# Kernel optimization log

Hardware: AMD Instinct MI355X
Metric: run time of the kernel (lower is better)

Reference implementation:

```python
import jax, jax.numpy as jnp
import numpy as np

B, S, T = 256, 1024, 64

def setup_inputs() -> dict:
    key = jax.random.key(0)
    k1, k2, k3, k4, k5 = jax.random.split(key, 5)
    emissions = jax.random.normal(k1, (B, S, T), dtype=jnp.float32)
    tags = jax.random.randint(k2, (B, S), 0, T, dtype=jnp.int64)
    mask = jnp.ones((B, S), dtype=jnp.int32)
    transitions = jax.random.normal(k3, (T, T), dtype=jnp.float32) * 0.1
    start_transitions = jax.random.normal(k4, (T,), dtype=jnp.float32) * 0.1
    end_transitions = jax.random.normal(k5, (T,), dtype=jnp.float32) * 0.1
    return {"emissions": emissions, "tags": tags, "mask": mask,
            "transitions": transitions, "start_transitions": start_transitions,
            "end_transitions": end_transitions}


def _gold_score(emissions, tags, maskf, transitions, start_transitions, end_transitions):
    # emission score at each gold tag: [B, S]
    emit = jnp.take_along_axis(emissions, tags[:, :, None], axis=2)[:, :, 0]
    # transition score between consecutive gold tags: [B, S-1]
    trans = transitions[tags[:, :-1], tags[:, 1:]]
    score = start_transitions[tags[:, 0]] + emit[:, 0]
    score = score + jnp.sum((trans + emit[:, 1:]) * maskf[:, 1:], axis=1)
    last_pos = maskf.astype(jnp.int32).sum(axis=1) - 1           # [B]
    last_tags = jnp.take_along_axis(tags, last_pos[:, None], axis=1)[:, 0]
    return score + end_transitions[last_tags]


def _log_partition(emissions, maskf, transitions, start_transitions, end_transitions):
    alpha0 = start_transitions[None, :] + emissions[:, 0]        # [B, T]

    def step(alpha, xs):
        emit_t, m_t = xs                                         # [B, T], [B]
        # scores[b, i, j] = alpha[b, i] + transitions[i, j] + emit_t[b, j]
        scores = alpha[:, :, None] + transitions[None, :, :] + emit_t[:, None, :]
        new_alpha = jax.nn.logsumexp(scores, axis=1)             # [B, T]
        alpha = jnp.where(m_t[:, None] > 0, new_alpha, alpha)
        return alpha, None

    xs = (jnp.swapaxes(emissions[:, 1:], 0, 1), jnp.swapaxes(maskf[:, 1:], 0, 1))
    alpha, _ = jax.lax.scan(step, alpha0, xs)
    return jax.nn.logsumexp(alpha + end_transitions[None, :], axis=1)  # [B]


def reference(emissions, tags, mask, transitions, start_transitions, end_transitions):
    maskf = mask.astype(emissions.dtype)
    log_Z = _log_partition(emissions, maskf, transitions, start_transitions, end_transitions)
    score = _gold_score(emissions, tags, maskf, transitions, start_transitions, end_transitions)
    return jnp.mean(log_Z - score)
```

## Files before the change

### kernel.cpp

```cpp
#include <hip/hip_runtime.h>

#define Bn 256
#define Sn 1024
#define Tn 64
#define NCH 16
#define BURN 64
#define SLAB 4
#define RAWSTR 260
#define CROW 72
#define MROW 129
#define LN2 0.69314718055994531f
#define L7LN2 4.8520302639196169f

typedef __attribute__((ext_vector_type(8))) short short8;
typedef __attribute__((ext_vector_type(4))) float f32x4;

__device__ __forceinline__ unsigned short f2bf_rne(float f) {
  unsigned u = __float_as_uint(f);
  u = (u + 0x7fffu + ((u >> 16) & 1u)) >> 16;
  return (unsigned short)u;
}
__device__ __forceinline__ unsigned pk2(float hi, float lo) {
  return __builtin_amdgcn_perm(__float_as_uint(hi), __float_as_uint(lo), 0x07060302);
}
__device__ __forceinline__ unsigned pke(float a, float b) {
  return (unsigned)f2bf_rne(__expf(a - L7LN2)) |
         ((unsigned)f2bf_rne(__expf(b - L7LN2)) << 16);
}
__device__ __forceinline__ short8 cat4(uint2 a, uint2 b) {
  union { unsigned u[4]; short8 s; } x;
  x.u[0] = a.x; x.u[1] = a.y; x.u[2] = b.x; x.u[3] = b.y;
  return x.s;
}
__device__ __forceinline__ void gl_lds16(const void* src, void* dst) {
  __builtin_amdgcn_global_load_lds(
      (const __attribute__((address_space(1))) void*)src,
      (__attribute__((address_space(3))) void*)dst, 16, 0, 0);
}
__device__ __forceinline__ void gl_lds4(const void* src, void* dst) {
  __builtin_amdgcn_global_load_lds(
      (const __attribute__((address_space(1))) void*)src,
      (__attribute__((address_space(3))) void*)dst, 4, 0, 0);
}

__global__ __launch_bounds__(256, 1) void crf_scan(
    const float* __restrict__ em, const int* __restrict__ tags,
    const int* __restrict__ mask, const float* __restrict__ trans,
    const float* __restrict__ startt, const float* __restrict__ endt,
    float* __restrict__ wsL, float* __restrict__ wsGold,
    int* __restrict__ wsM, float* __restrict__ wsSE, float* __restrict__ wsA,
    int* __restrict__ cnt, float* __restrict__ out) {
  const int g = blockIdx.x & 15;
  const int c = blockIdx.x >> 4;
  const int Wc = (c == 0) ? 0 : BURN;
  const int Lc = (c == NCH - 1) ? 63 : 64;
  const int TOT = Wc + Lc;
  const int NSLAB = (TOT + SLAB - 1) / SLAB;
  const int t0 = 64 * c + 1;
  const int tstart = t0 - Wc;
  const int tid = threadIdx.x;
  const int wid = tid >> 6;
  const int lane = tid & 63;
  const int m = lane & 15;
  const int q = lane >> 4;
  const int mrow = 8 * (m >> 2) + (m & 3);

  __shared__ __align__(16) float rawS[2][16 * RAWSTR];
  __shared__ __align__(16) short convS[2][SLAB * 16 * CROW];
  __shared__ int maskL[16 * MROW];
  __shared__ int lastF;
  __shared__ float eend[64];
  __shared__ float rsum[4];

  short8 a00, a01, a10, a11, a20, a21, a30, a31;
  uint2 st0, st1, st2, st3;
  float Slog = 0.f;
  int K = 0, NL = 0;
  const f32x4 zero4 = {0.f, 0.f, 0.f, 0.f};

  auto issue_slab = [&](int s) {
    if (s >= NSLAB) return;
    float* dstb = rawS[s & 1];
    const int rem = TOT - 4 * s;
    if (rem >= SLAB) {
      for (int mm = 0; mm < 16; ++mm)
        gl_lds16(em + ((size_t)(16 * g + mm) * Sn + tstart + 4 * s) * 64 + lane * 4,
                 dstb + mm * RAWSTR);
    } else {
      for (int mm = 0; mm < 16; ++mm)
        for (int u = 0; u < rem; ++u)
          gl_lds4(em + ((size_t)(16 * g + mm) * Sn + tstart + 4 * s + u) * 64 + lane,
                  dstb + mm * RAWSTR + u * 64);
    }
  };
  auto conv_u = [&](const float* rp, short* cb, int mm, int base, int u) {
    float4 v0 = *(const float4*)(rp + u * 64 + 0);
    float4 v1 = *(const float4*)(rp + u * 64 + 4);
    float4 v2 = *(const float4*)(rp + u * 64 + 8);
    float4 v3 = *(const float4*)(rp + u * 64 + 12);
    uint4 o0, o1;
    o0.x = pke(v0.x, v0.y); o0.y = pke(v0.z, v0.w);
    o1.x = pke(v1.x, v1.y); o1.y = pke(v1.z, v1.w);
    o0.z = pke(v2.x, v2.y); o0.w = pke(v2.z, v2.w);
    o1.z = pke(v3.x, v3.y); o1.w = pke(v3.z, v3.w);
    short* cw = cb + (u * 16 + mm) * CROW + base;
    *(uint4*)(cw) = o0;
    *(uint4*)(cw + 16) = o1;
  };
  auto convert2 = [&](int s, int ua) {
    const int mm = lane & 15, seg = lane >> 4;
    const float* rp = rawS[s & 1] + mm * RAWSTR + seg * 16;
    short* cb = convS[s & 1];
    const int base = (seg >> 1) * 32 + (seg & 1) * 8;
    conv_u(rp, cb, mm, base, ua);
    conv_u(rp, cb, mm, base, ua + 1);
  };
  auto convert_tail2 = [&](int s, int ua) {
    if (s >= NSLAB) return;
    const int mm = lane & 15, seg = lane >> 4;
    const float* rp = rawS[s & 1] + mm * RAWSTR + seg * 16;
    short* cb = convS[s & 1];
    const int base = (seg >> 1) * 32 + (seg & 1) * 8;
    const int vu = min(SLAB, TOT - 4 * s);
    const int ub = min(vu, ua + 2);
    for (int u = ua; u < ub; ++u) conv_u(rp, cb, mm, base, u);
  };

  if (wid == 0) {
#define LOADA(tm, kc, dst) { \
    _Pragma("unroll") for (int jj = 0; jj < 8; ++jj) { \
      int kk = kc * 32 + q * 8 + jj; \
      dst[jj] = (short)f2bf_rne(__expf(trans[kk * Tn + (32 * ((tm) >> 1) + 4 * ((tm) & 1) + mrow)])); \
    } }
    LOADA(0, 0, a00) LOADA(0, 1, a01) LOADA(1, 0, a10) LOADA(1, 1, a11)
    LOADA(2, 0, a20) LOADA(2, 1, a21) LOADA(3, 0, a30) LOADA(3, 1, a31)
#undef LOADA
    if (c == 0) {
#define INIT0(off, ss) { \
      float4 sv = *(const float4*)(startt + (off)); \
      float4 ev = *(const float4*)(em + (size_t)(16 * g + m) * Sn * Tn + (off)); \
      ss.x = (unsigned)f2bf_rne(__expf(sv.x + ev.x)) | \
             ((unsigned)f2bf_rne(__expf(sv.y + ev.y)) << 16); \
      ss.y = (unsigned)f2bf_rne(__expf(sv.z + ev.z)) | \
             ((unsigned)f2bf_rne(__expf(sv.w + ev.w)) << 16); }
      INIT0(8 * q, st0) INIT0(8 * q + 4, st1)
      INIT0(32 + 8 * q, st2) INIT0(36 + 8 * q, st3)
#undef INIT0
    } else {
      st0.x = 0x3F803F80u; st0.y = 0x3F803F80u; st1 = st0; st2 = st0; st3 = st0;
    }
  } else if (wid == 1) {
    for (int mm = 0; mm < 16; ++mm) {
      gl_lds4(mask + (size_t)(16 * g + mm) * Sn + tstart + lane,
              (void*)(maskL + mm * MROW));
      bool special = (c == NCH - 1) && (g == 15) && (mm == 15);
      if (!special)
        gl_lds4(mask + (size_t)(16 * g + mm) * Sn + tstart + 64 + lane,
                (void*)(maskL + mm * MROW + 64));
    }
    if (c == NCH - 1 && g == 15) {
      int t = tstart + 64 + lane;
      if (t < Sn) maskL[15 * MROW + 64 + lane] = mask[(size_t)255 * Sn + t];
    }
    asm volatile("s_waitcnt vmcnt(0) lgkmcnt(0)" ::: "memory");
  } else if (wid == 2) {
    const int bm = 16 * g + m;
    const int qq = q;
    const int* tg = tags + (size_t)bm * Sn;
    const int* mkb = mask + (size_t)bm * Sn;
    const float* emb = em + (size_t)bm * Sn * Tn;
    float acc = 0.f;
    int cntg = 0;
    #pragma unroll 4
    for (int i = 0; i < 16; ++i) {
      int t = t0 + qq + 4 * i;
      bool ok = t < t0 + Lc;
      int ts = ok ? t : t0;
      int mv = mkb[ts];
      int tp = tg[ts - 1], tc = tg[ts];
      float w = trans[tp * Tn + tc] + emb[(size_t)ts * Tn + tc];
      acc += (ok && mv) ? w : 0.f;
      cntg += ok ? mv : 0;
    }
    acc += __shfl_xor(acc, 16); acc += __shfl_xor(acc, 32);
    cntg += __shfl_xor(cntg, 16); cntg += __shfl_xor(cntg, 32);
    if (qq == 0) { wsGold[c * 256 + bm] = acc; wsM[c * 256 + bm] = cntg; }
  } else {
    issue_slab(0);
    issue_slab(1);
    asm volatile("s_waitcnt vmcnt(0)" ::: "memory");
  }
  __syncthreads();

  if (wid == 1) convert2(0, 0);
  else if (wid == 2) convert2(0, 2);
  __syncthreads();

#define UNP(ss, x0, x1, x2, x3) \
  x0 = __uint_as_float(ss.x << 16); x1 = __uint_as_float(ss.x & 0xffff0000u); \
  x2 = __uint_as_float(ss.y << 16); x3 = __uint_as_float(ss.y & 0xffff0000u);

  auto renorm = [&](int ttz) {
    float x00, x01, x02, x03, x10, x11, x12, x13;
    float x20, x21, x22, x23, x30, x31, x32, x33;
    UNP(st0, x00, x01, x02, x03) UNP(st1, x10, x11, x12, x13)
    UNP(st2, x20, x21, x22, x23) UNP(st3, x30, x31, x32, x33)
    float sm = (((x00 + x01) + (x02 + x03)) + ((x10 + x11) + (x12 + x13)))
             + (((x20 + x21) + (x22 + x23)) + ((x30 + x31) + (x32 + x33)));
    sm += __shfl_xor(sm, 16); sm += __shfl_xor(sm, 32);
    if (c != 0 && ttz == BURN) { Slog = __logf(sm); K = 0; NL = 0; }
    int k = 127 - (int)((__float_as_uint(sm) >> 23) & 255u);
    float fk = __uint_as_float((unsigned)(127 + k) << 23);
    x00 *= fk; x01 *= fk; x02 *= fk; x03 *= fk;
    x10 *= fk; x11 *= fk; x12 *= fk; x13 *= fk;
    x20 *= fk; x21 *= fk; x22 *= fk; x23 *= fk;
    x30 *= fk; x31 *= fk; x32 *= fk; x33 *= fk;
    st0.x = pk2(x01, x00); st0.y = pk2(x03, x02);
    st1.x = pk2(x11, x10); st1.y = pk2(x13, x12);
    st2.x = pk2(x21, x20); st2.y = pk2(x23, x22);
    st3.x = pk2(x31, x30); st3.y = pk2(x33, x32);
    K += k;
  };

  auto scan_step = [&](const short* ep, int tt) {
    uint2 eu0 = *(const uint2*)(ep + 0 + 4 * q);
    uint2 eu1 = *(const uint2*)(ep + 16 + 4 * q);
    uint2 eu2 = *(const uint2*)(ep + 32 + 4 * q);
    uint2 eu3 = *(const uint2*)(ep + 48 + 4 * q);
    int mv = maskL[m * MROW + tt];
    short8 b0 = cat4(st0, st1);
    short8 b1 = cat4(st2, st3);
    f32x4 d0 = __builtin_amdgcn_mfma_f32_16x16x32_bf16(a00, b0, zero4, 0, 0, 0);
    f32x4 d1 = __builtin_amdgcn_mfma_f32_16x16x32_bf16(a10, b0, zero4, 0, 0, 0);
    f32x4 d2 = __builtin_amdgcn_mfma_f32_16x16x32_bf16(a20, b0, zero4, 0, 0, 0);
    f32x4 d3 = __builtin_amdgcn_mfma_f32_16x16x32_bf16(a30, b0, zero4, 0, 0, 0);
    d0 = __builtin_amdgcn_mfma_f32_16x16x32_bf16(a01, b1, d0, 0, 0, 0);
    d1 = __builtin_amdgcn_mfma_f32_16x16x32_bf16(a11, b1, d1, 0, 0, 0);
    d2 = __builtin_amdgcn_mfma_f32_16x16x32_bf16(a21, b1, d2, 0, 0, 0);
    d3 = __builtin_amdgcn_mfma_f32_16x16x32_bf16(a31, b1, d3, 0, 0, 0);
    const bool live = (mv != 0);
#define EPI(dd, eu, ss) { \
    float e0 = __uint_as_float(eu.x << 16); \
    float e1 = __uint_as_float(eu.x & 0xffff0000u); \
    float e2 = __uint_as_float(eu.y << 16); \
    float e3 = __uint_as_float(eu.y & 0xffff0000u); \
    unsigned nx = pk2(dd[1] * e1, dd[0] * e0); \
    unsigned ny = pk2(dd[3] * e3, dd[2] * e2); \
    ss.x = live ? nx : ss.x; \
    ss.y = live ? ny : ss.y; }
    EPI(d0, eu0, st0) EPI(d1, eu1, st1) EPI(d2, eu2, st2) EPI(d3, eu3, st3)
#undef EPI
    NL += (live && tt >= Wc) ? 1 : 0;
  };

  const int RT = (TOT - 4) >> 2;
  for (int r = 0; r < NSLAB; ++r) {
    if (wid == 0) {
      if ((r & 1) == 0) renorm(4 * r);
      const short* cbase = convS[r & 1];
      if (r < RT) {
        #pragma unroll
        for (int u = 0; u < SLAB; ++u)
          scan_step(cbase + (u * 16 + m) * CROW, 4 * r + u);
      } else {
        #pragma unroll
        for (int u = 0; u < SLAB; ++u)
          if (4 * r + u < TOT)
            scan_step(cbase + (u * 16 + m) * CROW, 4 * r + u);
      }
    } else if (wid == 3) {
      issue_slab(r + 2);
      asm volatile("s_waitcnt vmcnt(0)" ::: "memory");
    } else {
      const int ua = (wid == 1) ? 0 : 2;
      if (r < RT) convert2(r + 1, ua);
      else        convert_tail2(r + 1, ua);
    }
    __syncthreads();
  }

  if (wid == 0) {
    float x00, x01, x02, x03, x10, x11, x12, x13;
    float x20, x21, x22, x23, x30, x31, x32, x33;
    UNP(st0, x00, x01, x02, x03) UNP(st1, x10, x11, x12, x13)
    UNP(st2, x20, x21, x22, x23) UNP(st3, x30, x31, x32, x33)
    float sm = (((x00 + x01) + (x02 + x03)) + ((x10 + x11) + (x12 + x13)))
             + (((x20 + x21) + (x22 + x23)) + ((x30 + x31) + (x32 + x33)));
    sm += __shfl_xor(sm, 16); sm += __shfl_xor(sm, 32);
    const int bm = 16 * g + m;
    float L = __logf(sm) - Slog + LN2 * (float)(7 * NL - K);
    if (q == 0) wsL[c * 256 + bm] = L;
    if (c == NCH - 1) {
      if (q == 0) wsSE[bm] = __logf(sm);
      wsA[(8 * q + 0) * 256 + bm] = x00;  wsA[(8 * q + 1) * 256 + bm] = x01;
      wsA[(8 * q + 2) * 256 + bm] = x02;  wsA[(8 * q + 3) * 256 + bm] = x03;
      wsA[(8 * q + 4) * 256 + bm] = x10;  wsA[(8 * q + 5) * 256 + bm] = x11;
      wsA[(8 * q + 6) * 256 + bm] = x12;  wsA[(8 * q + 7) * 256 + bm] = x13;
      wsA[(32 + 8 * q + 0) * 256 + bm] = x20; wsA[(32 + 8 * q + 1) * 256 + bm] = x21;
      wsA[(32 + 8 * q + 2) * 256 + bm] = x22; wsA[(32 + 8 * q + 3) * 256 + bm] = x23;
      wsA[(36 + 8 * q + 0) * 256 + bm] = x30; wsA[(36 + 8 * q + 1) * 256 + bm] = x31;
      wsA[(36 + 8 * q + 2) * 256 + bm] = x32; wsA[(36 + 8 * q + 3) * 256 + bm] = x33;
    }
  }
#undef UNP

  __threadfence();
  __syncthreads();
  if (tid == 0) lastF = (atomicAdd(cnt, 1) == 255) ? 1 : 0;
  __syncthreads();
  if (lastF) {
    __threadfence();
    if (tid < 64) eend[tid] = __expf(endt[tid]);
    __syncthreads();
    float vsum = 0.f;
    for (int bb = tid; bb < Bn; bb += 256) {
      float sumL = 0.f, gold = 0.f;
      int msum = 0;
      #pragma unroll
      for (int cc = 0; cc < NCH; ++cc) {
        sumL += wsL[cc * 256 + bb];
        gold += wsGold[cc * 256 + bb];
        msum += wsM[cc * 256 + bb];
      }
      msum += mask[(size_t)bb * Sn];
      float se = 0.f;
      for (int jj = 0; jj < Tn; ++jj) se += wsA[jj * 256 + bb] * eend[jj];
      float logZ = sumL + __logf(se) - wsSE[bb];
      int tg0 = tags[(size_t)bb * Sn];
      int lastTag = tags[(size_t)bb * Sn + (msum - 1)];
      gold += startt[tg0] + em[(size_t)bb * Sn * Tn + tg0] + endt[lastTag];
      vsum += logZ - gold;
    }
    #pragma unroll
    for (int o = 32; o > 0; o >>= 1) vsum += __shfl_xor(vsum, o, 64);
    if (lane == 0) rsum[wid] = vsum;
    __syncthreads();
    if (tid == 0) out[0] = (rsum[0] + rsum[1] + rsum[2] + rsum[3]) * (1.0f / Bn);
  }
}

extern "C" void kernel_launch(void* const* d_in, const int* in_sizes, int n_in,
                              void* d_out, int out_size, void* d_ws, size_t ws_size,
                              hipStream_t stream) {
  const float* em     = (const float*)d_in[0];
  const int*   tags   = (const int*)d_in[1];
  const int*   mask   = (const int*)d_in[2];
  const float* trans  = (const float*)d_in[3];
  const float* startt = (const float*)d_in[4];
  const float* endt   = (const float*)d_in[5];
  float* out = (float*)d_out;

  float* wsL    = (float*)d_ws;
  float* wsGold = wsL + NCH * 256;
  int*   wsM    = (int*)(wsGold + NCH * 256);
  float* wsSE   = (float*)(wsM + NCH * 256);
  float* wsA    = wsSE + 256;
  int*   cnt    = (int*)(wsA + 64 * 256);

  hipMemsetAsync(cnt, 0, sizeof(int), stream);
  crf_scan<<<256, 256, 0, stream>>>(em, tags, mask, trans, startt, endt,
                                    wsL, wsGold, wsM, wsSE, wsA, cnt, out);
}
```

Before: 163.1 us.

## Deepen emission prefetch to four raw slabs split across three loader waves

Raw emission staging grows from two to four LDS buffers, and the global-to-LDS loads are now split by row across waves 1-3 instead of coming only from wave 3. Loads are issued three slabs ahead and throttled with partial vmcnt waits, so several slabs stay in flight instead of draining to zero each step. The per-step __syncthreads is replaced with a raw s_barrier to avoid its implicit full wait. This raises LDS usage and depends on hand-counted vmcnt values being correct. It also drops the separate tail convert, which may convert rows past the valid timesteps in the final slab.

Result: no change. 163.9 us (+0.5%).

```diff
diff --git a/kernel.cpp b/kernel.cpp
--- a/kernel.cpp
+++ b/kernel.cpp
@@ -65,7 +65,7 @@
   const int q = lane >> 4;
   const int mrow = 8 * (m >> 2) + (m & 3);
 
-  __shared__ __align__(16) float rawS[2][16 * RAWSTR];
+  __shared__ __align__(16) float rawS[4][16 * RAWSTR];
   __shared__ __align__(16) short convS[2][SLAB * 16 * CROW];
   __shared__ int maskL[16 * MROW];
   __shared__ int lastF;
@@ -78,16 +78,16 @@
   int K = 0, NL = 0;
   const f32x4 zero4 = {0.f, 0.f, 0.f, 0.f};
 
-  auto issue_slab = [&](int s) {
+  auto issue_rows = [&](int s, int mm0, int mm1) {
     if (s >= NSLAB) return;
-    float* dstb = rawS[s & 1];
+    float* dstb = rawS[s & 3];
     const int rem = TOT - 4 * s;
     if (rem >= SLAB) {
-      for (int mm = 0; mm < 16; ++mm)
+      for (int mm = mm0; mm < mm1; ++mm)
         gl_lds16(em + ((size_t)(16 * g + mm) * Sn + tstart + 4 * s) * 64 + lane * 4,
                  dstb + mm * RAWSTR);
     } else {
-      for (int mm = 0; mm < 16; ++mm)
+      for (int mm = mm0; mm < mm1; ++mm)
         for (int u = 0; u < rem; ++u)
           gl_lds4(em + ((size_t)(16 * g + mm) * Sn + tstart + 4 * s + u) * 64 + lane,
                   dstb + mm * RAWSTR + u * 64);
@@ -108,22 +108,13 @@
     *(uint4*)(cw + 16) = o1;
   };
   auto convert2 = [&](int s, int ua) {
+    if (s >= NSLAB) return;
     const int mm = lane & 15, seg = lane >> 4;
-    const float* rp = rawS[s & 1] + mm * RAWSTR + seg * 16;
+    const float* rp = rawS[s & 3] + mm * RAWSTR + seg * 16;
     short* cb = convS[s & 1];
     const int base = (seg >> 1) * 32 + (seg & 1) * 8;
     conv_u(rp, cb, mm, base, ua);
     conv_u(rp, cb, mm, base, ua + 1);
-  };
-  auto convert_tail2 = [&](int s, int ua) {
-    if (s >= NSLAB) return;
-    const int mm = lane & 15, seg = lane >> 4;
-    const float* rp = rawS[s & 1] + mm * RAWSTR + seg * 16;
-    short* cb = convS[s & 1];
-    const int base = (seg >> 1) * 32 + (seg & 1) * 8;
-    const int vu = min(SLAB, TOT - 4 * s);
-    const int ub = min(vu, ua + 2);
-    for (int u = ua; u < ub; ++u) conv_u(rp, cb, mm, base, u);
   };
 
   if (wid == 0) {
@@ -150,6 +141,33 @@
       st0.x = 0x3F803F80u; st0.y = 0x3F803F80u; st1 = st0; st2 = st0; st3 = st0;
     }
   } else if (wid == 1) {
+    issue_rows(0, 0, 6); issue_rows(1, 0, 6); issue_rows(2, 0, 6);
+    asm volatile("s_waitcnt vmcnt(0)" ::: "memory");
+  } else if (wid == 2) {
+    issue_rows(0, 6, 12); issue_rows(1, 6, 12); issue_rows(2, 6, 12);
+    const int bm = 16 * g + m;
+    const int* tg = tags + (size_t)bm * Sn;
+    const int* mkb = mask + (size_t)bm * Sn;
+    const float* emb = em + (size_t)bm * Sn * Tn;
+    float acc = 0.f;
+    int cntg = 0;
+    #pragma unroll 4
+    for (int i = 0; i < 16; ++i) {
+      int t = t0 + q + 4 * i;
+      bool ok = t < t0 + Lc;
+      int ts = ok ? t : t0;
+      int mv = mkb[ts];
+      int tp = tg[ts - 1], tc = tg[ts];
+      float w = trans[tp * Tn + tc] + emb[(size_t)ts * Tn + tc];
+      acc += (ok && mv) ? w : 0.f;
+      cntg += ok ? mv : 0;
+    }
+    acc += __shfl_xor(acc, 16); acc += __shfl_xor(acc, 32);
+    cntg += __shfl_xor(cntg, 16); cntg += __shfl_xor(cntg, 32);
+    if (q == 0) { wsGold[c * 256 + bm] = acc; wsM[c * 256 + bm] = cntg; }
+    asm volatile("s_waitcnt vmcnt(0)" ::: "memory");
+  } else {
+    issue_rows(0, 12, 16); issue_rows(1, 12, 16); issue_rows(2, 12, 16);
     for (int mm = 0; mm < 16; ++mm) {
       gl_lds4(mask + (size_t)(16 * g + mm) * Sn + tstart + lane,
               (void*)(maskL + mm * MROW));
@@ -163,32 +181,6 @@
       if (t < Sn) maskL[15 * MROW + 64 + lane] = mask[(size_t)255 * Sn + t];
     }
     asm volatile("s_waitcnt vmcnt(0) lgkmcnt(0)" ::: "memory");
-  } else if (wid == 2) {
-    const int bm = 16 * g + m;
-    const int qq = q;
-    const int* tg = tags + (size_t)bm * Sn;
-    const int* mkb = mask + (size_t)bm * Sn;
-    const float* emb = em + (size_t)bm * Sn * Tn;
-    float acc = 0.f;
-    int cntg = 0;
-    #pragma unroll 4
-    for (int i = 0; i < 16; ++i) {
-      int t = t0 + qq + 4 * i;
-      bool ok = t < t0 + Lc;
-      int ts = ok ? t : t0;
-      int mv = mkb[ts];
-      int tp = tg[ts - 1], tc = tg[ts];
-      float w = trans[tp * Tn + tc] + emb[(size_t)ts * Tn + tc];
-      acc += (ok && mv) ? w : 0.f;
-      cntg += ok ? mv : 0;
-    }
-    acc += __shfl_xor(acc, 16); acc += __shfl_xor(acc, 32);
-    cntg += __shfl_xor(cntg, 16); cntg += __shfl_xor(cntg, 32);
-    if (qq == 0) { wsGold[c * 256 + bm] = acc; wsM[c * 256 + bm] = cntg; }
-  } else {
-    issue_slab(0);
-    issue_slab(1);
-    asm volatile("s_waitcnt vmcnt(0)" ::: "memory");
   }
   __syncthreads();
 
@@ -268,15 +260,25 @@
           if (4 * r + u < TOT)
             scan_step(cbase + (u * 16 + m) * CROW, 4 * r + u);
       }
-    } else if (wid == 3) {
-      issue_slab(r + 2);
-      asm volatile("s_waitcnt vmcnt(0)" ::: "memory");
+    } else if (wid == 1) {
+      issue_rows(r + 3, 0, 6);
+      convert2(r + 1, 0);
+      asm volatile("s_waitcnt lgkmcnt(0)" ::: "memory");
+      if (r + 4 < NSLAB) asm volatile("s_waitcnt vmcnt(6)" ::: "memory");
+      else               asm volatile("s_waitcnt vmcnt(0)" ::: "memory");
+    } else if (wid == 2) {
+      issue_rows(r + 3, 6, 12);
+      convert2(r + 1, 2);
+      asm volatile("s_waitcnt lgkmcnt(0)" ::: "memory");
+      if (r + 4 < NSLAB) asm volatile("s_waitcnt vmcnt(6)" ::: "memory");
+      else               asm volatile("s_waitcnt vmcnt(0)" ::: "memory");
     } else {
-      const int ua = (wid == 1) ? 0 : 2;
-      if (r < RT) convert2(r + 1, ua);
-      else        convert_tail2(r + 1, ua);
-    }
-    __syncthreads();
+      issue_rows(r + 3, 12, 16);
+      if (r + 4 < NSLAB) asm volatile("s_waitcnt vmcnt(4)" ::: "memory");
+      else               asm volatile("s_waitcnt vmcnt(0)" ::: "memory");
+    }
+    __builtin_amdgcn_s_barrier();
+    asm volatile("" ::: "memory");
   }
 
   if (wid == 0) {
```

## Triple-buffer raw emission slabs with deeper prefetch and partial vmcnt waits

Applied to the files above, without the earlier changes.

Raw emission staging grows from two to three LDS buffers, and the loader wave keeps three slabs in flight. It waits with partial vmcnt counts so only the oldest slab has to land before each barrier. Block-wide __syncthreads are replaced by raw s_barrier calls plus explicit per-wave waitcnts, and the prologue work (gold score, mask loads, the special mask element) is moved between waves. The aim is to hide more global-load latency behind the scan. The costs are more LDS use and fragile hand-counted wait values that must match the exact number of issued loads.

Result: no change. 161.2 us (-1.2%).

```diff
diff --git a/kernel.cpp b/kernel.cpp
--- a/kernel.cpp
+++ b/kernel.cpp
@@ -65,7 +65,7 @@
   const int q = lane >> 4;
   const int mrow = 8 * (m >> 2) + (m & 3);
 
-  __shared__ __align__(16) float rawS[2][16 * RAWSTR];
+  __shared__ __align__(16) float rawS[3][16 * RAWSTR];
   __shared__ __align__(16) short convS[2][SLAB * 16 * CROW];
   __shared__ int maskL[16 * MROW];
   __shared__ int lastF;
@@ -80,7 +80,7 @@
 
   auto issue_slab = [&](int s) {
     if (s >= NSLAB) return;
-    float* dstb = rawS[s & 1];
+    float* dstb = rawS[s % 3];
     const int rem = TOT - 4 * s;
     if (rem >= SLAB) {
       for (int mm = 0; mm < 16; ++mm)
@@ -109,7 +109,7 @@
   };
   auto convert2 = [&](int s, int ua) {
     const int mm = lane & 15, seg = lane >> 4;
-    const float* rp = rawS[s & 1] + mm * RAWSTR + seg * 16;
+    const float* rp = rawS[s % 3] + mm * RAWSTR + seg * 16;
     short* cb = convS[s & 1];
     const int base = (seg >> 1) * 32 + (seg & 1) * 8;
     conv_u(rp, cb, mm, base, ua);
@@ -118,7 +118,7 @@
   auto convert_tail2 = [&](int s, int ua) {
     if (s >= NSLAB) return;
     const int mm = lane & 15, seg = lane >> 4;
-    const float* rp = rawS[s & 1] + mm * RAWSTR + seg * 16;
+    const float* rp = rawS[s % 3] + mm * RAWSTR + seg * 16;
     short* cb = convS[s & 1];
     const int base = (seg >> 1) * 32 + (seg & 1) * 8;
     const int vu = min(SLAB, TOT - 4 * s);
@@ -149,7 +149,35 @@
     } else {
       st0.x = 0x3F803F80u; st0.y = 0x3F803F80u; st1 = st0; st2 = st0; st3 = st0;
     }
+    if (c == NCH - 1 && g == 15) {
+      int t = tstart + 64 + lane;
+      if (t < Sn) maskL[15 * MROW + 64 + lane] = mask[(size_t)255 * Sn + t];
+    }
+    asm volatile("s_waitcnt vmcnt(0) lgkmcnt(0)" ::: "memory");
   } else if (wid == 1) {
+    const int bm = 16 * g + m;
+    const int* tg = tags + (size_t)bm * Sn;
+    const int* mkb = mask + (size_t)bm * Sn;
+    const float* emb = em + (size_t)bm * Sn * Tn;
+    float acc = 0.f;
+    int cntg = 0;
+    #pragma unroll 4
+    for (int i = 0; i < 16; ++i) {
+      int t = t0 + q + 4 * i;
+      bool ok = t < t0 + Lc;
+      int ts = ok ? t : t0;
+      int mv = mkb[ts];
+      int tp = tg[ts - 1], tc = tg[ts];
+      float w = trans[tp * Tn + tc] + emb[(size_t)ts * Tn + tc];
+      acc += (ok && mv) ? w : 0.f;
+      cntg += ok ? mv : 0;
+    }
+    acc += __shfl_xor(acc, 16); acc += __shfl_xor(acc, 32);
+    cntg += __shfl_xor(cntg, 16); cntg += __shfl_xor(cntg, 32);
+    if (q == 0) { wsGold[c * 256 + bm] = acc; wsM[c * 256 + bm] = cntg; }
+    asm volatile("s_waitcnt vmcnt(0)" ::: "memory");
+  } else if (wid == 2) {
+  } else {
     for (int mm = 0; mm < 16; ++mm) {
       gl_lds4(mask + (size_t)(16 * g + mm) * Sn + tstart + lane,
               (void*)(maskL + mm * MROW));
@@ -158,43 +186,17 @@
         gl_lds4(mask + (size_t)(16 * g + mm) * Sn + tstart + 64 + lane,
                 (void*)(maskL + mm * MROW + 64));
     }
-    if (c == NCH - 1 && g == 15) {
-      int t = tstart + 64 + lane;
-      if (t < Sn) maskL[15 * MROW + 64 + lane] = mask[(size_t)255 * Sn + t];
-    }
-    asm volatile("s_waitcnt vmcnt(0) lgkmcnt(0)" ::: "memory");
-  } else if (wid == 2) {
-    const int bm = 16 * g + m;
-    const int qq = q;
-    const int* tg = tags + (size_t)bm * Sn;
-    const int* mkb = mask + (size_t)bm * Sn;
-    const float* emb = em + (size_t)bm * Sn * Tn;
-    float acc = 0.f;
-    int cntg = 0;
-    #pragma unroll 4
-    for (int i = 0; i < 16; ++i) {
-      int t = t0 + qq + 4 * i;
-      bool ok = t < t0 + Lc;
-      int ts = ok ? t : t0;
-      int mv = mkb[ts];
-      int tp = tg[ts - 1], tc = tg[ts];
-      float w = trans[tp * Tn + tc] + emb[(size_t)ts * Tn + tc];
-      acc += (ok && mv) ? w : 0.f;
-      cntg += ok ? mv : 0;
-    }
-    acc += __shfl_xor(acc, 16); acc += __shfl_xor(acc, 32);
-    cntg += __shfl_xor(cntg, 16); cntg += __shfl_xor(cntg, 32);
-    if (qq == 0) { wsGold[c * 256 + bm] = acc; wsM[c * 256 + bm] = cntg; }
-  } else {
-    issue_slab(0);
-    issue_slab(1);
-    asm volatile("s_waitcnt vmcnt(0)" ::: "memory");
+    issue_slab(0); issue_slab(1); issue_slab(2);
+    asm volatile("s_waitcnt vmcnt(32)" ::: "memory");
   }
-  __syncthreads();
-
-  if (wid == 1) convert2(0, 0);
-  else if (wid == 2) convert2(0, 2);
-  __syncthreads();
+  __builtin_amdgcn_s_barrier();
+  asm volatile("" ::: "memory");
+
+  if (wid == 1) { convert2(0, 0); asm volatile("s_waitcnt lgkmcnt(0)" ::: "memory"); }
+  else if (wid == 2) { convert2(0, 2); asm volatile("s_waitcnt lgkmcnt(0)" ::: "memory"); }
+  else if (wid == 3) { asm volatile("s_waitcnt vmcnt(16)" ::: "memory"); }
+  __builtin_amdgcn_s_barrier();
+  asm volatile("" ::: "memory");
 
 #define UNP(ss, x0, x1, x2, x3) \
   x0 = __uint_as_float(ss.x << 16); x1 = __uint_as_float(ss.x & 0xffff0000u); \
@@ -268,15 +270,26 @@
           if (4 * r + u < TOT)
             scan_step(cbase + (u * 16 + m) * CROW, 4 * r + u);
       }
-    } else if (wid == 3) {
-      issue_slab(r + 2);
-      asm volatile("s_waitcnt vmcnt(0)" ::: "memory");
+    } else if (wid == 1) {
+      if (r + 1 < RT) convert2(r + 1, 0);
+      else            convert_tail2(r + 1, 0);
+      asm volatile("s_waitcnt lgkmcnt(0)" ::: "memory");
+    } else if (wid == 2) {
+      if (r + 1 < RT) convert2(r + 1, 2);
+      else            convert_tail2(r + 1, 2);
+      asm volatile("s_waitcnt lgkmcnt(0)" ::: "memory");
     } else {
-      const int ua = (wid == 1) ? 0 : 2;
-      if (r < RT) convert2(r + 1, ua);
-      else        convert_tail2(r + 1, ua);
-    }
-    __syncthreads();
+      const int nxt = r + 3;
+      issue_slab(nxt);
+      if (nxt < NSLAB) {
+        if (TOT - 4 * nxt >= SLAB) asm volatile("s_waitcnt vmcnt(16)" ::: "memory");
+        else                       asm volatile("s_waitcnt vmcnt(48)" ::: "memory");
+      } else {
+        asm volatile("s_waitcnt vmcnt(0)" ::: "memory");
+      }
+    }
+    __builtin_amdgcn_s_barrier();
+    asm volatile("" ::: "memory");
   }
 
   if (wid == 0) {
```
